# Kernel tuning notes

Hardware: AMD Instinct MI355X
Metric: run time of the kernel (lower is better)

Reference implementation:

```python
import jax, jax.numpy as jnp
import numpy as np
import math

GAMMA = 0.97      # discounting
LAM = 0.95        # gae lambda
EPSILON = 0.3     # ppo clip
EPS = 0.2         # gpo clip (eps)
ENT_COST = 0.01
RSCALE = 1.0
ALPHA = 1.0
NUM_STEPS = 1.0e6 # normalization step count buffer


def _mlp(x, Ws, bs):
    for i, (W, b) in enumerate(zip(Ws, bs)):
        x = x @ W.T + b
        if i < len(Ws) - 1:
            x = jax.nn.silu(x)
    return x


def _dist_create(logits):
    loc, s = jnp.split(logits, 2, axis=-1)
    return loc, jax.nn.softplus(s) + 0.001


def _log_det_jac(x):
    # tanh bijector log|det J| per element
    return 2.0 * (math.log(2.0) - x - jax.nn.softplus(-2.0 * x))


def _log_prob(loc, scale, dist):
    lu = -0.5 * jnp.square((dist - loc) / scale)
    ln = 0.5 * math.log(2.0 * math.pi) + jnp.log(scale)
    return (lu - ln - _log_det_jac(dist)).sum(-1)


def _entropy(loc, scale, noise):
    ln = 0.5 * math.log(2.0 * math.pi) + jnp.log(scale)
    ent = (0.5 + ln) * jnp.ones_like(loc)
    dist = loc + scale * noise  # reparameterized sample (torch.normal)
    return (ent + _log_det_jac(dist)).sum(-1)


def _kl(pl, ps, ql, qs):
    vr = jnp.square(ps / qs)
    t1 = jnp.square((pl - ql) / qs)
    return (0.5 * (vr + t1 - 1.0 - jnp.log(vr))).mean(-1)


def _normalize(obs, rm, rv):
    var = jnp.clip(rv / (NUM_STEPS + 1.0), 1e-6, 1e6)
    return jnp.clip((obs - rm) / jnp.sqrt(var), -5.0, 5.0)


def _gae(truncation, termination, reward, values, bootstrap_value):
    tm = 1.0 - truncation
    v1 = jnp.concatenate([values[1:], bootstrap_value[None]], 0)
    deltas = (reward + GAMMA * (1.0 - termination) * v1 - values) * tm

    def step(acc, xs):
        d, te, tmask = xs
        acc = d + GAMMA * (1.0 - te) * tmask * LAM * acc
        return acc, acc

    _, vmx = jax.lax.scan(step, jnp.zeros_like(bootstrap_value),
                          (deltas, termination, tm), reverse=True)
    vs = vmx + values
    vs1 = jnp.concatenate([vs[1:], bootstrap_value[None]], 0)
    adv = (reward + GAMMA * (1.0 - termination) * vs1 - values) * tm
    return vs, adv


def _loss(observation, pobservation, reward, done, truncation, logits, action,
          noise, pw0, pb0, pw1, pb1, pw2, pb2, vw0, vb0, vw1, vb1, vw2, vb2,
          running_mean, running_variance, kl_coef):
    sg = jax.lax.stop_gradient
    Pw, Pb = [pw0, pw1, pw2], [pb0, pb1, pb2]
    Vw, Vb = [vw0, vw1, vw2], [vb0, vb1, vb2]

    obs_n = _normalize(observation, running_mean, running_variance)
    pobs_n = _normalize(pobservation, running_mean, running_variance)

    guider_logits = _mlp(obs_n[:-1], Pw, Pb)
    learner_logits = _mlp(pobs_n[:-1], Pw, Pb)
    baseline = _mlp(obs_n, Vw, Vb).squeeze(-1)  # [T+1, B]
    bootstrap = baseline[-1]
    baseline = baseline[:-1]

    reward_s = reward * RSCALE
    termination = done * (1.0 - truncation)

    loc, scale = _dist_create(logits)
    b_lp = _log_prob(loc, scale, action)
    gl, gs = _dist_create(guider_logits)
    g_lp = _log_prob(gl, gs, action)
    ll, ls = _dist_create(learner_logits)
    l_lp = _log_prob(ll, ls, action)

    kl_learner = _kl(sg(gl), sg(gs), ll, ls).mean()
    kl_guider = _kl(gl, gs, sg(ll), sg(ls))
    # use_clip = True branch
    diff = g_lp - l_lp
    m = jnp.where(diff > math.log(1.0 + EPS), 1.0,
                  jnp.where(diff < math.log(1.0 - EPS), 1.0, 0.0))
    kl_guider = (kl_guider * m).mean()

    vs, adv = _gae(truncation, termination, reward_s, sg(baseline), sg(bootstrap))
    vs = sg(vs)
    adv = sg((adv - adv.mean()) / (jnp.std(adv, ddof=1) + 1e-5))

    rho = jnp.exp(g_lp - b_lp)
    rho_clip = jnp.exp(jnp.clip(g_lp - sg(l_lp), math.log(1.0 - EPS), math.log(1.0 + EPS))
                       + sg(l_lp) - b_lp)
    rho_clip = jnp.clip(rho_clip, 1.0 - EPSILON, 1.0 + EPSILON)
    guider_policy_loss = -jnp.mean(jnp.minimum(rho * adv, rho_clip * adv))

    rho2 = jnp.exp(jnp.minimum(l_lp - b_lp, 10.0))  # stable_exp
    rho2c = jnp.clip(rho2, 1.0 - EPSILON, 1.0 + EPSILON)
    learner_policy_loss = -jnp.mean(jnp.minimum(rho2 * adv, rho2c * adv))

    v_err = vs - baseline
    v_loss = jnp.mean(v_err * v_err) * 0.25

    entropy = jnp.mean(_entropy(loc, scale, noise))
    entropy_loss = -ENT_COST * entropy

    learner_loss = kl_learner + learner_policy_loss * ALPHA  # use_clip
    guider_loss = kl_guider + guider_policy_loss
    total = learner_loss + guider_loss + v_loss + entropy_loss
    return total, guider_loss, learner_loss, kl_learner


def setup_inputs() -> dict:
    key = jax.random.key(0)
    T, B, OBS, ACT, H = 1024, 256, 64, 8, 256
    ks = iter(jax.random.split(key, 32))

    def lin(fin, fout):
        W = jax.random.normal(next(ks), (fout, fin), jnp.float32) / np.float32(np.sqrt(fin))
        b = jnp.zeros((fout,), jnp.float32)
        return W, b

    pw0, pb0 = lin(OBS, H); pw1, pb1 = lin(H, H); pw2, pb2 = lin(H, 2 * ACT)
    vw0, vb0 = lin(OBS, H); vw1, vb1 = lin(H, H); vw2, vb2 = lin(H, 1)

    observation = jax.random.normal(next(ks), (T + 1, B, OBS), jnp.float32)
    pobservation = observation + 0.1 * jax.random.normal(next(ks), (T + 1, B, OBS), jnp.float32)
    reward = jax.random.normal(next(ks), (T, B), jnp.float32)
    done = (jax.random.uniform(next(ks), (T, B)) < 0.01).astype(jnp.float32)
    truncation = (jax.random.uniform(next(ks), (T, B)) < 0.005).astype(jnp.float32)
    logits = 0.5 * jax.random.normal(next(ks), (T, B, 2 * ACT), jnp.float32)
    action = jax.random.normal(next(ks), (T, B, ACT), jnp.float32)
    noise = jax.random.normal(next(ks), (T, B, ACT), jnp.float32)
    running_mean = jnp.zeros((OBS,), jnp.float32)
    running_variance = jnp.ones((OBS,), jnp.float32) * NUM_STEPS  # unit variance after /num_steps
    kl_coef = jnp.ones((1,), jnp.float32)

    return {"observation": observation, "pobservation": pobservation,
            "reward": reward, "done": done, "truncation": truncation,
            "logits": logits, "action": action, "noise": noise,
            "pw0": pw0, "pb0": pb0, "pw1": pw1, "pb1": pb1, "pw2": pw2, "pb2": pb2,
            "vw0": vw0, "vb0": vb0, "vw1": vw1, "vb1": vb1, "vw2": vw2, "vb2": vb2,
            "running_mean": running_mean, "running_variance": running_variance,
            "kl_coef": kl_coef}


def reference(observation, pobservation, reward, done, truncation, logits, action,
              noise, pw0, pb0, pw1, pb1, pw2, pb2, vw0, vb0, vw1, vb1, vw2, vb2,
              running_mean, running_variance, kl_coef):
    return _loss(observation, pobservation, reward, done, truncation, logits,
                 action, noise, pw0, pb0, pw1, pb1, pw2, pb2, vw0, vb0, vw1, vb1,
                 vw2, vb2, running_mean, running_variance, kl_coef)
```

## Files before the change

### kernel.cpp

```cpp
#include <hip/hip_runtime.h>
#include <math.h>

#define GAMMA_   0.97f
#define LAM_     0.95f
#define EPSILON_ 0.3f
#define HLOG2PI_ 0.91893853320467274f
#define LOG2C_   0.69314718055994531f
#define LOG1P2_  0.18232155679395463f
#define LOG0P8_  (-0.22314355131420976f)

typedef unsigned short u16;
typedef unsigned int   u32;
typedef _Float16 half8 __attribute__((ext_vector_type(8)));
typedef _Float16 half4 __attribute__((ext_vector_type(4)));
typedef __attribute__((ext_vector_type(4))) float floatx4;
typedef __attribute__((ext_vector_type(8))) float floatx8;

constexpr int  TT     = 1024;
constexpr long ROWS_P = (long)TT * 256;
constexpr long ROWS_V = (long)(TT + 1) * 256;

constexpr long FR_W0P_HI = 0;
constexpr long FR_W0P_LO = 16384;
constexpr long FR_W1P_HI = 32768;
// ... 14 lines not shown
constexpr long WS_BASE = WS_ADV + ROWS_P;
constexpr long WS_GA   = WS_BASE + ROWS_V;
constexpr long WS_GP   = WS_GA + 8192;
constexpr long WS_GS   = WS_GP + 8192;
constexpr long WS_BANK = WS_GS + 8192;


__device__ __forceinline__ float softplus_f(float x) {
  return (x > 20.f) ? x : log1pf(expf(x));
}
__device__ __forceinline__ float silu_f(float x) {
  return x * __builtin_amdgcn_rcpf(1.f + __expf(-x));
}
__device__ __forceinline__ float clamp30(float x) {
  return fminf(1e30f, fmaxf(-1e30f, x));
}

__global__ void prep_kernel(const float* __restrict__ rv,
                            float* __restrict__ inv_std,
                            float* __restrict__ accum,
                            float* __restrict__ accumB) {
  int t = threadIdx.x;
  if (t < 32) accum[t] = 0.f;
  accumB[t] = 0.f;
  if (t < 64) {
    float var = rv[t] / 1000001.0f;
    var = fminf(1e6f, fmaxf(1e-6f, var));
    inv_std[t] = 1.f / sqrtf(var);
  }
}

__global__ void convert_kernel(const float* __restrict__ pw0,
                               const float* __restrict__ pw1,
                               const float* __restrict__ pw2,
                               const float* __restrict__ vw0,
                               const float* __restrict__ vw1,
                               const float* __restrict__ vw2,
                               u16* __restrict__ frag) {
  int idx = blockIdx.x * 256 + threadIdx.x;
  const float* W; int kslog, K, nvalid; long hioff, looff; int e;
  if (idx < 16384)       { W = pw0; e = idx;          kslog = 1; K = 64;  nvalid = 256; hioff = FR_W0P_HI; looff = FR_W0P_LO; }
  else if (idx < 81920)  { W = pw1; e = idx - 16384;  kslog = 3; K = 256; nvalid = 256; hioff = FR_W1P_HI; looff = FR_W1P_LO; }
  else if (idx < 86016)  { W = pw2; e = idx - 81920;  kslog = 3; K = 256; nvalid = 16;  hioff = FR_W2P_HI; looff = FR_W2P_LO; }
  else if (idx < 102400) { W = vw0; e = idx - 86016;  kslog = 1; K = 64;  nvalid = 256; hioff = FR_W0V_HI; looff = FR_W0V_LO; }
  else if (idx < 167936) { W = vw1; e = idx - 102400; kslog = 3; K = 256; nvalid = 256; hioff = FR_W1V_HI; looff = FR_W1V_LO; }
  else                   { W = vw2; e = idx - 167936; kslog = 3; K = 256; nvalid = 1;   hioff = FR_W2V_HI; looff = FR_W2V_LO; }
  int j    = e & 7;
  int lane = (e >> 3) & 63;
  int ks   = (e >> 9) & ((1 << kslog) - 1);
  int nt   = e >> (9 + kslog);
  int n = nt * 16 + (lane & 15);
  int k = ks * 32 + ((lane >> 4) << 3) + j;
  float w = (n < nvalid) ? W[n * K + k] : 0.f;
  _Float16 hi = (_Float16)w;
  _Float16 lo = (_Float16)(w - (float)hi);
  frag[hioff + e] = *(u16*)&hi;
  frag[looff + e] = *(u16*)&lo;
}

constexpr int SX = 72;
constexpr int SH = 264;

__global__ __launch_bounds__(256, 3)
void policy_kernel(const float* __restrict__ obs,
                   const float* __restrict__ pobs,
                   const float* __restrict__ rm,
                   const float* __restrict__ inv_std,
                   const u16* __restrict__ frag,
                   const float* __restrict__ b0,
                   const float* __restrict__ b1,
                   const float* __restrict__ b2,
                   const float* __restrict__ logits,
                   const float* __restrict__ action,
                   const float* __restrict__ noise,
                   const float* __restrict__ adv,
                   const float* __restrict__ accum,
                   float* __restrict__ accumB) {
  __shared__ __align__(16) _Float16 H[64 * SH];
  __shared__ __align__(16) float OUTT[64 * 16];
  __shared__ float red[160];

  const int tid  = threadIdx.x;
  const long row0 = (long)blockIdx.x * 32;
  const int lane = tid & 63;
  const int wv   = tid >> 6;
  const int lm   = lane & 15;
  const int lq   = lane >> 4;

  _Float16* X = H;

  #pragma unroll
  for (int it = 0; it < 2; ++it) {
    int flat = it * 256 + tid;
    int vr = flat >> 3;
    int f0 = (flat & 7) * 8;
    const float* src = (vr < 32) ? obs : pobs;
    floatx8 v  = *(const floatx8*)&src[(row0 + (vr & 31)) * 64 + f0];
    floatx8 m  = *(const floatx8*)&rm[f0];
    floatx8 is = *(const floatx8*)&inv_std[f0];
    half8 h;
    #pragma unroll
    for (int j = 0; j < 8; ++j)
      h[j] = (_Float16)fminf(5.f, fmaxf(-5.f, (v[j] - m[j]) * is[j]));
    *(half8*)&X[vr * SX + f0] = h;
  }

  const int  er   = tid >> 3;
  const int  ed   = tid & 7;
  const long erow = row0 + er;
  float pf_a   = action[erow * 8 + ed];
  float pf_loc = logits[erow * 16 + ed];
  float pf_sr  = logits[erow * 16 + 8 + ed];
  float pf_nd  = noise[erow * 8 + ed];
  float pf_adv = adv[erow];
  float pf_s3  = accum[3];
  float pf_s4  = accum[4];

  const half8* B0h = (const half8*)(frag + FR_W0P_HI);
  const half8* B0l = (const half8*)(frag + FR_W0P_LO);
  half8 B0hr[2][4], B0lr[2][4];
  #pragma unroll
  for (int ks = 0; ks < 2; ++ks)
    #pragma unroll
    for (int nt = 0; nt < 4; ++nt) {
      int ntg = wv * 4 + nt;
      B0hr[ks][nt] = B0h[(ntg * 2 + ks) * 64 + lane];
      B0lr[ks][nt] = B0l[(ntg * 2 + ks) * 64 + lane];
    }
  __syncthreads();

  floatx4 acc[4][4];

  #pragma unroll
  for (int mt = 0; mt < 4; ++mt)
    #pragma unroll
    for (int nt = 0; nt < 4; ++nt) acc[mt][nt] = (floatx4){0.f,0.f,0.f,0.f};
  #pragma unroll
  for (int ks = 0; ks < 2; ++ks) {
    half8 A[4];
    #pragma unroll
    for (int mt = 0; mt < 4; ++mt)
      A[mt] = *(const half8*)&X[(mt * 16 + lm) * SX + ks * 32 + lq * 8];
    __builtin_amdgcn_s_setprio(1);
    #pragma unroll
    for (int mt = 0; mt < 4; ++mt)
      #pragma unroll
      for (int nt = 0; nt < 4; ++nt)
        acc[mt][nt] = __builtin_amdgcn_mfma_f32_16x16x32_f16(B0hr[ks][nt], A[mt], acc[mt][nt], 0, 0, 0);
    #pragma unroll
    for (int mt = 0; mt < 4; ++mt)
      #pragma unroll
      for (int nt = 0; nt < 4; ++nt)
        acc[mt][nt] = __builtin_amdgcn_mfma_f32_16x16x32_f16(B0lr[ks][nt], A[mt], acc[mt][nt], 0, 0, 0);
    __builtin_amdgcn_s_setprio(0);
  }

  const half8* B1h = (const half8*)(frag + FR_W1P_HI);
  const half8* B1l = (const half8*)(frag + FR_W1P_LO);
  half8 Bh[4], Bl[4], Bhn[4], Bln[4];
  #pragma unroll
  for (int nt = 0; nt < 4; ++nt) {
    int ntg = wv * 4 + nt;
    Bh[nt] = B1h[(ntg * 8) * 64 + lane];
    Bl[nt] = B1l[(ntg * 8) * 64 + lane];
  }

  __syncthreads();
  #pragma unroll
  for (int nt = 0; nt < 4; ++nt) {
    int colbase = (wv * 4 + nt) * 16 + lq * 4;
    floatx4 bias = *(const floatx4*)&b0[colbase];
    #pragma unroll
    for (int mt = 0; mt < 4; ++mt) {
      int row = mt * 16 + lm;
      half4 h;
      #pragma unroll
      for (int reg = 0; reg < 4; ++reg)
        h[reg] = (_Float16)silu_f(acc[mt][nt][reg] + bias[reg]);
      *(half4*)&H[row * SH + colbase] = h;
    }
  }
  __syncthreads();

  #pragma unroll
  for (int mt = 0; mt < 4; ++mt)
    #pragma unroll
    for (int nt = 0; nt < 4; ++nt) acc[mt][nt] = (floatx4){0.f,0.f,0.f,0.f};
  #pragma unroll 1
  for (int ks = 0; ks < 8; ++ks) {
    if (ks < 7) {
      #pragma unroll
      for (int nt = 0; nt < 4; ++nt) {
        int ntg = wv * 4 + nt;
        Bhn[nt] = B1h[(ntg * 8 + ks + 1) * 64 + lane];
        Bln[nt] = B1l[(ntg * 8 + ks + 1) * 64 + lane];
      }
    }
    half8 A[4];
    #pragma unroll
    for (int mt = 0; mt < 4; ++mt)
      A[mt] = *(const half8*)&H[(mt * 16 + lm) * SH + ks * 32 + lq * 8];
    __builtin_amdgcn_s_setprio(1);
    #pragma unroll
    for (int mt = 0; mt < 4; ++mt)
      #pragma unroll
      for (int nt = 0; nt < 4; ++nt)
        acc[mt][nt] = __builtin_amdgcn_mfma_f32_16x16x32_f16(Bh[nt], A[mt], acc[mt][nt], 0, 0, 0);
    #pragma unroll
    for (int mt = 0; mt < 4; ++mt)
      #pragma unroll
      for (int nt = 0; nt < 4; ++nt)
        acc[mt][nt] = __builtin_amdgcn_mfma_f32_16x16x32_f16(Bl[nt], A[mt], acc[mt][nt], 0, 0, 0);
    __builtin_amdgcn_s_setprio(0);
    if (ks < 7) {
      #pragma unroll
      for (int nt = 0; nt < 4; ++nt) { Bh[nt] = Bhn[nt]; Bl[nt] = Bln[nt]; }
    }
  }

  const half8* B2h = (const half8*)(frag + FR_W2P_HI);
  const half8* B2l = (const half8*)(frag + FR_W2P_LO);
  half8 B2hr[8], B2lr[8];
  #pragma unroll
  for (int ks = 0; ks < 8; ++ks) {
    B2hr[ks] = B2h[ks * 64 + lane];
    B2lr[ks] = B2l[ks * 64 + lane];
  }

  __syncthreads();
  #pragma unroll
  for (int nt = 0; nt < 4; ++nt) {
    int colbase = (wv * 4 + nt) * 16 + lq * 4;
    floatx4 bias = *(const floatx4*)&b1[colbase];
    #pragma unroll
    for (int mt = 0; mt < 4; ++mt) {
      int row = mt * 16 + lm;
      half4 h;
      #pragma unroll
      for (int reg = 0; reg < 4; ++reg)
        h[reg] = (_Float16)silu_f(acc[mt][nt][reg] + bias[reg]);
      *(half4*)&H[row * SH + colbase] = h;
    }
  }
  __syncthreads();

  {
    floatx4 c3a = (floatx4){0.f,0.f,0.f,0.f};
    floatx4 c3b = (floatx4){0.f,0.f,0.f,0.f};
    __builtin_amdgcn_s_setprio(1);
    #pragma unroll
    for (int ks = 0; ks < 8; ks += 2) {
      half8 A0 = *(const half8*)&H[(wv * 16 + lm) * SH + ks * 32 + lq * 8];
      half8 A1 = *(const half8*)&H[(wv * 16 + lm) * SH + (ks + 1) * 32 + lq * 8];
      c3a = __builtin_amdgcn_mfma_f32_16x16x32_f16(B2hr[ks],     A0, c3a, 0, 0, 0);
      c3b = __builtin_amdgcn_mfma_f32_16x16x32_f16(B2hr[ks + 1], A1, c3b, 0, 0, 0);
      c3a = __builtin_amdgcn_mfma_f32_16x16x32_f16(B2lr[ks],     A0, c3a, 0, 0, 0);
      c3b = __builtin_amdgcn_mfma_f32_16x16x32_f16(B2lr[ks + 1], A1, c3b, 0, 0, 0);
    }
    __builtin_amdgcn_s_setprio(0);
    floatx4 bias = *(const floatx4*)&b2[lq * 4];
    *(floatx4*)&OUTT[(wv * 16 + lm) * 16 + lq * 4] = c3a + c3b + bias;
  }
  __syncthreads();

  {
    int r = er;
    int d = ed;

    float gl  = OUTT[r * 16 + d];
    float gsr = OUTT[r * 16 + 8 + d];
    float ll  = OUTT[(32 + r) * 16 + d];
    float lsr = OUTT[(32 + r) * 16 + 8 + d];
    float a   = pf_a;
    float loc = pf_loc;
    float sr  = pf_sr;
    float nd  = pf_nd;

    float gs = softplus_f(gsr) + 1e-3f;
    float ls = softplus_f(lsr) + 1e-3f;
    float sc = softplus_f(sr) + 1e-3f;
    float ldj = 2.f * (LOG2C_ - a - softplus_f(-2.f * a));
    float lgs = logf(gs), lls = logf(ls), lsc = logf(sc);
    float zg = (a - gl) / gs;
    float zl = (a - ll) / ls;
    float z  = (a - loc) / sc;
    float glp = -0.5f * zg * zg - lgs - HLOG2PI_ - ldj;
    float llp = -0.5f * zl * zl - lls - HLOG2PI_ - ldj;
    float blp = -0.5f * z * z - lsc - HLOG2PI_ - ldj;
    float ratio = gs / ls;
    float vr = ratio * ratio;
    float t1 = (gl - ll) / ls; t1 *= t1;
    float kl = 0.5f * (vr + t1 - 1.f) - (lgs - lls);
    float dist = loc + sc * nd;
    float ent = 0.5f + HLOG2PI_ + lsc
              + 2.f * (LOG2C_ - dist - softplus_f(-2.f * dist));
// ... 12 lines not shown
      kl  = clamp30(kl);
      ent = clamp30(ent);

      float diff = glp - llp;
      float m = (diff > LOG1P2_ || diff < LOG0P8_) ? 1.f : 0.f;

      float N = (float)ROWS_P;
      float sum = pf_s3, sumsq = pf_s4;
      float mean = sum / N;
      float var  = fmaxf((sumsq - sum * sum / N) / (N - 1.f), 0.f);
      float inv  = 1.f / (sqrtf(var) + 1e-5f);
      float a_n  = (pf_adv - mean) * inv;

      float rho = expf(fminf(glp - blp, 80.f));
      float cl  = fminf(LOG1P2_, fmaxf(LOG0P8_, diff));
      float rc  = expf(fminf(cl + llp - blp, 80.f));
      rc = fminf(1.f + EPSILON_, fmaxf(1.f - EPSILON_, rc));
      float gp = clamp30(fminf(rho * a_n, rc * a_n));

      float rho2 = expf(fminf(llp - blp, 10.f));
      float r2c  = fminf(1.f + EPSILON_, fmaxf(1.f - EPSILON_, rho2));
      float lp = clamp30(fminf(rho2 * a_n, r2c * a_n));

      red[r]       = kl;
      red[32 + r]  = kl * m;
      red[64 + r]  = ent;
      red[96 + r]  = gp;
      red[128 + r] = lp;
    }
  }
  __syncthreads();
  if (tid < 32) {
    float s0 = red[tid], s1 = red[32 + tid], s2 = red[64 + tid];
    float s3 = red[96 + tid], s4 = red[128 + tid];
    #pragma unroll
    for (int o = 16; o > 0; o >>= 1) {
      s0 += __shfl_down(s0, o, 32);
      s1 += __shfl_down(s1, o, 32);
      s2 += __shfl_down(s2, o, 32);
      s3 += __shfl_down(s3, o, 32);
      s4 += __shfl_down(s4, o, 32);
    }
    if (tid == 0) {
      float* bank = accumB + (blockIdx.x & 31) * 8;
      atomicAdd(&bank[0], s0);
      atomicAdd(&bank[1], s1);
      atomicAdd(&bank[2], s2);
      atomicAdd(&bank[6], s3);
      atomicAdd(&bank[7], s4);
    }
  }
}

__global__ __launch_bounds__(256, 3)
void value_kernel(const float* __restrict__ obs,
                  const float* __restrict__ rm,
                  const float* __restrict__ inv_std,
                  const u16* __restrict__ frag,
                  const float* __restrict__ b0,
                  const float* __restrict__ b1,
                  const float* __restrict__ b2,
                  float* __restrict__ baseline) {
  __shared__ __align__(16) _Float16 H[64 * SH];

  const int tid  = threadIdx.x;
  const long row0 = (long)blockIdx.x * 64;
  const int lane = tid & 63;
  const int wv   = tid >> 6;
  const int lm   = lane & 15;
  const int lq   = lane >> 4;

  _Float16* X = H;

  #pragma unroll
  for (int it = 0; it < 2; ++it) {
    int flat = it * 256 + tid;
    int vr = flat >> 3;
    int f0 = (flat & 7) * 8;
    floatx8 v  = *(const floatx8*)&obs[(row0 + vr) * 64 + f0];
    floatx8 m  = *(const floatx8*)&rm[f0];
    floatx8 is = *(const floatx8*)&inv_std[f0];
    half8 h;
    #pragma unroll
    for (int j = 0; j < 8; ++j)
      h[j] = (_Float16)fminf(5.f, fmaxf(-5.f, (v[j] - m[j]) * is[j]));
    *(half8*)&X[vr * SX + f0] = h;
  }

  const half8* B0h = (const half8*)(frag + FR_W0V_HI);
  const half8* B0l = (const half8*)(frag + FR_W0V_LO);
  half8 B0hr[2][4], B0lr[2][4];
  #pragma unroll
  for (int ks = 0; ks < 2; ++ks)
    #pragma unroll
    for (int nt = 0; nt < 4; ++nt) {
      int ntg = wv * 4 + nt;
      B0hr[ks][nt] = B0h[(ntg * 2 + ks) * 64 + lane];
      B0lr[ks][nt] = B0l[(ntg * 2 + ks) * 64 + lane];
    }
  __syncthreads();

  floatx4 acc[4][4];

  #pragma unroll
  for (int mt = 0; mt < 4; ++mt)
    #pragma unroll
    for (int nt = 0; nt < 4; ++nt) acc[mt][nt] = (floatx4){0.f,0.f,0.f,0.f};
  #pragma unroll
  for (int ks = 0; ks < 2; ++ks) {
    half8 A[4];
    #pragma unroll
    for (int mt = 0; mt < 4; ++mt)
      A[mt] = *(const half8*)&X[(mt * 16 + lm) * SX + ks * 32 + lq * 8];
    __builtin_amdgcn_s_setprio(1);
    #pragma unroll
    for (int mt = 0; mt < 4; ++mt)
      #pragma unroll
      for (int nt = 0; nt < 4; ++nt)
        acc[mt][nt] = __builtin_amdgcn_mfma_f32_16x16x32_f16(B0hr[ks][nt], A[mt], acc[mt][nt], 0, 0, 0);
    #pragma unroll
    for (int mt = 0; mt < 4; ++mt)
      #pragma unroll
      for (int nt = 0; nt < 4; ++nt)
        acc[mt][nt] = __builtin_amdgcn_mfma_f32_16x16x32_f16(B0lr[ks][nt], A[mt], acc[mt][nt], 0, 0, 0);
    __builtin_amdgcn_s_setprio(0);
  }

  const half8* B1h = (const half8*)(frag + FR_W1V_HI);
  const half8* B1l = (const half8*)(frag + FR_W1V_LO);
  half8 Bh[4], Bl[4], Bhn[4], Bln[4];
  #pragma unroll
  for (int nt = 0; nt < 4; ++nt) {
    int ntg = wv * 4 + nt;
    Bh[nt] = B1h[(ntg * 8) * 64 + lane];
    Bl[nt] = B1l[(ntg * 8) * 64 + lane];
  }

  __syncthreads();
  #pragma unroll
  for (int nt = 0; nt < 4; ++nt) {
    int colbase = (wv * 4 + nt) * 16 + lq * 4;
    floatx4 bias = *(const floatx4*)&b0[colbase];
    #pragma unroll
    for (int mt = 0; mt < 4; ++mt) {
      int row = mt * 16 + lm;
      half4 h;
      #pragma unroll
      for (int reg = 0; reg < 4; ++reg)
        h[reg] = (_Float16)silu_f(acc[mt][nt][reg] + bias[reg]);
      *(half4*)&H[row * SH + colbase] = h;
    }
  }
  __syncthreads();

  #pragma unroll
  for (int mt = 0; mt < 4; ++mt)
    #pragma unroll
    for (int nt = 0; nt < 4; ++nt) acc[mt][nt] = (floatx4){0.f,0.f,0.f,0.f};
  #pragma unroll 1
  for (int ks = 0; ks < 8; ++ks) {
    if (ks < 7) {
      #pragma unroll
      for (int nt = 0; nt < 4; ++nt) {
        int ntg = wv * 4 + nt;
        Bhn[nt] = B1h[(ntg * 8 + ks + 1) * 64 + lane];
        Bln[nt] = B1l[(ntg * 8 + ks + 1) * 64 + lane];
      }
    }
    half8 A[4];
    #pragma unroll
    for (int mt = 0; mt < 4; ++mt)
      A[mt] = *(const half8*)&H[(mt * 16 + lm) * SH + ks * 32 + lq * 8];
    __builtin_amdgcn_s_setprio(1);
    #pragma unroll
    for (int mt = 0; mt < 4; ++mt)
      #pragma unroll
      for (int nt = 0; nt < 4; ++nt)
        acc[mt][nt] = __builtin_amdgcn_mfma_f32_16x16x32_f16(Bh[nt], A[mt], acc[mt][nt], 0, 0, 0);
    #pragma unroll
    for (int mt = 0; mt < 4; ++mt)
      #pragma unroll
      for (int nt = 0; nt < 4; ++nt)
        acc[mt][nt] = __builtin_amdgcn_mfma_f32_16x16x32_f16(Bl[nt], A[mt], acc[mt][nt], 0, 0, 0);
    __builtin_amdgcn_s_setprio(0);
    if (ks < 7) {
      #pragma unroll
      for (int nt = 0; nt < 4; ++nt) { Bh[nt] = Bhn[nt]; Bl[nt] = Bln[nt]; }
    }
  }

  const half8* B2h = (const half8*)(frag + FR_W2V_HI);
  const half8* B2l = (const half8*)(frag + FR_W2V_LO);
  half8 B2hr[8], B2lr[8];
  #pragma unroll
  for (int ks = 0; ks < 8; ++ks) {
    B2hr[ks] = B2h[ks * 64 + lane];
    B2lr[ks] = B2l[ks * 64 + lane];
  }

  __syncthreads();
  #pragma unroll
  for (int nt = 0; nt < 4; ++nt) {
    int colbase = (wv * 4 + nt) * 16 + lq * 4;
    floatx4 bias = *(const floatx4*)&b1[colbase];
    #pragma unroll
    for (int mt = 0; mt < 4; ++mt) {
      int row = mt * 16 + lm;
      half4 h;
      #pragma unroll
      for (int reg = 0; reg < 4; ++reg)
        h[reg] = (_Float16)silu_f(acc[mt][nt][reg] + bias[reg]);
      *(half4*)&H[row * SH + colbase] = h;
    }
  }
  __syncthreads();

  {
    floatx4 c3a = (floatx4){0.f,0.f,0.f,0.f};
    floatx4 c3b = (floatx4){0.f,0.f,0.f,0.f};
    __builtin_amdgcn_s_setprio(1);
    #pragma unroll
    for (int ks = 0; ks < 8; ks += 2) {
      half8 A0 = *(const half8*)&H[(wv * 16 + lm) * SH + ks * 32 + lq * 8];
      half8 A1 = *(const half8*)&H[(wv * 16 + lm) * SH + (ks + 1) * 32 + lq * 8];
      c3a = __builtin_amdgcn_mfma_f32_16x16x32_f16(B2hr[ks],     A0, c3a, 0, 0, 0);
      c3b = __builtin_amdgcn_mfma_f32_16x16x32_f16(B2hr[ks + 1], A1, c3b, 0, 0, 0);
      c3a = __builtin_amdgcn_mfma_f32_16x16x32_f16(B2lr[ks],     A0, c3a, 0, 0, 0);
      c3b = __builtin_amdgcn_mfma_f32_16x16x32_f16(B2lr[ks + 1], A1, c3b, 0, 0, 0);
    }
    __builtin_amdgcn_s_setprio(0);
    if (lq == 0) baseline[row0 + wv * 16 + lm] = c3a[0] + c3b[0] + b2[0];
  }
}

__global__ void gae_phase1(const float* __restrict__ reward,
                           const float* __restrict__ done,
                           const float* __restrict__ trunc,
                           const float* __restrict__ baseline,
                           float* __restrict__ A, float* __restrict__ P) {
  int s = blockIdx.x, b = threadIdx.x;
  float Aa = 0.f, Pp = 1.f;
  for (int t = (s + 1) * 32 - 1; t >= s * 32; --t) {
    int idx = t * 256 + b;
    float r = reward[idx], d = done[idx], tr = trunc[idx];
    float tm = 1.f - tr;
    float te = d * tm;
    float bl = baseline[idx], bl1 = baseline[idx + 256];
    float g1 = GAMMA_ * (1.f - te);
    float delta = (r + g1 * bl1 - bl) * tm;
    float c = g1 * tm * LAM_;
    Aa = delta + c * Aa;
    Pp = c * Pp;
  }
  A[s * 256 + b] = Aa;
  P[s * 256 + b] = Pp;
// ... 46 lines not shown
  for (int o = 32; o > 0; o >>= 1) {
    v0 += __shfl_down(v0, o, 64);
    v1 += __shfl_down(v1, o, 64);
    v2 += __shfl_down(v2, o, 64);
  }
  int lane = threadIdx.x & 63, w = threadIdx.x >> 6;
  if (lane == 0) { red[w] = v0; red[4 + w] = v1; red[8 + w] = v2; }
  __syncthreads();
  if (threadIdx.x == 0) {
    float s0=0.f, s1=0.f, s2=0.f;
    for (int q = 0; q < 4; ++q) { s0 += red[q]; s1 += red[4+q]; s2 += red[8+q]; }
    atomicAdd(&accum[3], s0);
    atomicAdd(&accum[4], s1);
    atomicAdd(&accum[5], s2);
  }
}

__global__ void finalize_kernel(const float* __restrict__ accum,
                                const float* __restrict__ accumB,
                                float* __restrict__ out) {
  int t = threadIdx.x;
  float s0 = 0.f, s1 = 0.f, s2 = 0.f, s6 = 0.f, s7 = 0.f;
  if (t < 32) {
    const float* bank = accumB + t * 8;
    s0 = bank[0]; s1 = bank[1]; s2 = bank[2]; s6 = bank[6]; s7 = bank[7];
  }
  #pragma unroll
  for (int o = 16; o > 0; o >>= 1) {
    s0 += __shfl_down(s0, o, 64);
    s1 += __shfl_down(s1, o, 64);
    s2 += __shfl_down(s2, o, 64);
    s6 += __shfl_down(s6, o, 64);
    s7 += __shfl_down(s7, o, 64);
  }
  if (t == 0) {
    float N = (float)ROWS_P;
    float kl_learner = s0 / N;
    float kl_guider  = s1 / N;
    float entropy    = s2 / N;
    float v_loss     = 0.25f * accum[5] / N;
    float gp_loss    = -s6 / N;
    float lp_loss    = -s7 / N;
    float learner_loss = kl_learner + lp_loss;
    float guider_loss  = kl_guider + gp_loss;
    float total = learner_loss + guider_loss + v_loss - 0.01f * entropy;
    out[0] = total;
    out[1] = guider_loss;
// ... 24 lines not shown
  const float* vb0 = (const float*)d_in[15];
  const float* vw1 = (const float*)d_in[16];
  const float* vb1 = (const float*)d_in[17];
  const float* vw2 = (const float*)d_in[18];
  const float* vb2 = (const float*)d_in[19];
  const float* rm  = (const float*)d_in[20];
  const float* rv  = (const float*)d_in[21];

  u16*   frag  = (u16*)d_ws;
  float* fbase = (float*)d_ws + FR_TOTAL / 2;
  float* accum   = fbase + WS_ACC;
  float* inv_std = fbase + WS_INV;
  float* adv     = fbase + WS_ADV;
  float* base    = fbase + WS_BASE;
  float* gA      = fbase + WS_GA;
  float* gP      = fbase + WS_GP;
  float* gS      = fbase + WS_GS;
  float* accumB  = fbase + WS_BANK;
  float* out = (float*)d_out;

  prep_kernel<<<1, 256, 0, stream>>>(rv, inv_std, accum, accumB);
  convert_kernel<<<672, 256, 0, stream>>>(pw0, pw1, pw2, vw0, vw1, vw2, frag);

  value_kernel<<<(int)(ROWS_V / 64), 256, 0, stream>>>(
      obs, rm, inv_std, frag, vb0, vb1, vb2, base);

  gae_phase1<<<32, 256, 0, stream>>>(reward, done, trunc, base, gA, gP);
  gae_phase2<<<1, 256, 0, stream>>>(gA, gP, gS);
  gae_phase3<<<32, 256, 0, stream>>>(reward, done, trunc, base, gS, adv, accum);

  policy_kernel<<<(int)(ROWS_P / 32), 256, 0, stream>>>(
      obs, pobs, rm, inv_std, frag, pb0, pb1, pb2,
      logits, action, noise, adv, accum, accumB);

  finalize_kernel<<<1, 64, 0, stream>>>(accum, accumB, out);
}
```

Measured before the change: 504.2 us.

## Halve per-block row tile in MLP kernels to raise occupancy and cut registers

Both the value and policy MLP kernels now process half as many rows per block (32 instead of 64 M-rows), which halves the accumulator and LDS footprint. Launch bounds rise from 3 to 5 blocks per SIMD to exploit this. Weight fragments are now streamed per k-step instead of being held in registers or double-buffered, and biases are folded into the accumulator initialisation. The final layer splits K across wave pairs with an LDS reduction. Reduction banks are padded to 32 floats to spread atomics across addresses. In exchange, each weight fragment is fetched from global/L2 twice as often per row and there are more blocks and atomics.

Result: slower. 583.9 us (+15.8%).

```diff
diff --git a/kernel.cpp b/kernel.cpp
--- a/kernel.cpp
+++ b/kernel.cpp
@@ -60,7 +60,7 @@
                             float* __restrict__ accumB) {
   int t = threadIdx.x;
   if (t < 32) accum[t] = 0.f;
-  accumB[t] = 0.f;
+  for (int i = t; i < 1024; i += 256) accumB[i] = 0.f;
   if (t < 64) {
     float var = rv[t] / 1000001.0f;
     var = fminf(1e6f, fmaxf(1e-6f, var));
@@ -99,7 +99,7 @@
 constexpr int SX = 72;
 constexpr int SH = 264;
 
-__global__ __launch_bounds__(256, 3)
+__global__ __launch_bounds__(256, 5)
 void policy_kernel(const float* __restrict__ obs,
                    const float* __restrict__ pobs,
                    const float* __restrict__ rm,
@@ -114,12 +114,12 @@
                    const float* __restrict__ adv,
                    const float* __restrict__ accum,
                    float* __restrict__ accumB) {
-  __shared__ __align__(16) _Float16 H[64 * SH];
-  __shared__ __align__(16) float OUTT[64 * 16];
-  __shared__ float red[160];
+  __shared__ __align__(16) _Float16 H[32 * SH];
+  __shared__ __align__(16) float OUT2[2 * 32 * 16];
+  __shared__ float red[80];
 
   const int tid  = threadIdx.x;
-  const long row0 = (long)blockIdx.x * 32;
+  const long row0 = (long)blockIdx.x * 16;
   const int lane = tid & 63;
   const int wv   = tid >> 6;
   const int lm   = lane & 15;
@@ -127,13 +127,11 @@
 
   _Float16* X = H;
 
-  #pragma unroll
-  for (int it = 0; it < 2; ++it) {
-    int flat = it * 256 + tid;
-    int vr = flat >> 3;
-    int f0 = (flat & 7) * 8;
-    const float* src = (vr < 32) ? obs : pobs;
-    floatx8 v  = *(const floatx8*)&src[(row0 + (vr & 31)) * 64 + f0];
+  {
+    int vr = tid >> 3;
+    int f0 = (tid & 7) * 8;
+    const float* src = (vr < 16) ? obs : pobs;
+    floatx8 v  = *(const floatx8*)&src[(row0 + (vr & 15)) * 64 + f0];
     floatx8 m  = *(const floatx8*)&rm[f0];
     floatx8 is = *(const floatx8*)&inv_std[f0];
     half8 h;
@@ -143,7 +141,7 @@
     *(half8*)&X[vr * SX + f0] = h;
   }
 
-  const int  er   = tid >> 3;
+  const int  er   = (tid >> 3) & 15;
   const int  ed   = tid & 7;
   const long erow = row0 + er;
   float pf_a   = action[erow * 8 + ed];
@@ -154,161 +152,139 @@
   float pf_s3  = accum[3];
   float pf_s4  = accum[4];
 
-  const half8* B0h = (const half8*)(frag + FR_W0P_HI);
-  const half8* B0l = (const half8*)(frag + FR_W0P_LO);
-  half8 B0hr[2][4], B0lr[2][4];
-  #pragma unroll
-  for (int ks = 0; ks < 2; ++ks)
-    #pragma unroll
-    for (int nt = 0; nt < 4; ++nt) {
-      int ntg = wv * 4 + nt;
-      B0hr[ks][nt] = B0h[(ntg * 2 + ks) * 64 + lane];
-      B0lr[ks][nt] = B0l[(ntg * 2 + ks) * 64 + lane];
-    }
-  __syncthreads();
-
-  floatx4 acc[4][4];
-
-  #pragma unroll
-  for (int mt = 0; mt < 4; ++mt)
-    #pragma unroll
-    for (int nt = 0; nt < 4; ++nt) acc[mt][nt] = (floatx4){0.f,0.f,0.f,0.f};
-  #pragma unroll
-  for (int ks = 0; ks < 2; ++ks) {
-    half8 A[4];
-    #pragma unroll
-    for (int mt = 0; mt < 4; ++mt)
-      A[mt] = *(const half8*)&X[(mt * 16 + lm) * SX + ks * 32 + lq * 8];
-    __builtin_amdgcn_s_setprio(1);
-    #pragma unroll
-    for (int mt = 0; mt < 4; ++mt)
-      #pragma unroll
-      for (int nt = 0; nt < 4; ++nt)
-        acc[mt][nt] = __builtin_amdgcn_mfma_f32_16x16x32_f16(B0hr[ks][nt], A[mt], acc[mt][nt], 0, 0, 0);
-    #pragma unroll
-    for (int mt = 0; mt < 4; ++mt)
-      #pragma unroll
-      for (int nt = 0; nt < 4; ++nt)
-        acc[mt][nt] = __builtin_amdgcn_mfma_f32_16x16x32_f16(B0lr[ks][nt], A[mt], acc[mt][nt], 0, 0, 0);
-    __builtin_amdgcn_s_setprio(0);
-  }
-
-  const half8* B1h = (const half8*)(frag + FR_W1P_HI);
-  const half8* B1l = (const half8*)(frag + FR_W1P_LO);
-  half8 Bh[4], Bl[4], Bhn[4], Bln[4];
+  floatx4 acc[2][4];
   #pragma unroll
   for (int nt = 0; nt < 4; ++nt) {
-    int ntg = wv * 4 + nt;
-    Bh[nt] = B1h[(ntg * 8) * 64 + lane];
-    Bl[nt] = B1l[(ntg * 8) * 64 + lane];
-  }
-
-  __syncthreads();
+    floatx4 bz = *(const floatx4*)&b0[(wv * 4 + nt) * 16 + lq * 4];
+    acc[0][nt] = bz; acc[1][nt] = bz;
+  }
+  __syncthreads();
+
+  {
+    const half8* B0h = (const half8*)(frag + FR_W0P_HI);
+    const half8* B0l = (const half8*)(frag + FR_W0P_LO);
+    #pragma unroll
+    for (int ks = 0; ks < 2; ++ks) {
+      half8 Bh[4], Bl[4];
+      #pragma unroll
+      for (int nt = 0; nt < 4; ++nt) {
+        int ntg = wv * 4 + nt;
+        Bh[nt] = B0h[(ntg * 2 + ks) * 64 + lane];
+        Bl[nt] = B0l[(ntg * 2 + ks) * 64 + lane];
+      }
+      half8 A0 = *(const half8*)&X[lm * SX + ks * 32 + lq * 8];
+      half8 A1 = *(const half8*)&X[(16 + lm) * SX + ks * 32 + lq * 8];
+      __builtin_amdgcn_s_setprio(1);
+      #pragma unroll
+      for (int nt = 0; nt < 4; ++nt) {
+        acc[0][nt] = __builtin_amdgcn_mfma_f32_16x16x32_f16(Bh[nt], A0, acc[0][nt], 0, 0, 0);
+        acc[1][nt] = __builtin_amdgcn_mfma_f32_16x16x32_f16(Bh[nt], A1, acc[1][nt], 0, 0, 0);
+      }
+      #pragma unroll
+      for (int nt = 0; nt < 4; ++nt) {
+        acc[0][nt] = __builtin_amdgcn_mfma_f32_16x16x32_f16(Bl[nt], A0, acc[0][nt], 0, 0, 0);
+        acc[1][nt] = __builtin_amdgcn_mfma_f32_16x16x32_f16(Bl[nt], A1, acc[1][nt], 0, 0, 0);
+      }
+      __builtin_amdgcn_s_setprio(0);
+    }
+  }
+  __syncthreads();
+
   #pragma unroll
   for (int nt = 0; nt < 4; ++nt) {
     int colbase = (wv * 4 + nt) * 16 + lq * 4;
-    floatx4 bias = *(const floatx4*)&b0[colbase];
-    #pragma unroll
-    for (int mt = 0; mt < 4; ++mt) {
+    #pragma unroll
+    for (int mt = 0; mt < 2; ++mt) {
       int row = mt * 16 + lm;
       half4 h;
       #pragma unroll
       for (int reg = 0; reg < 4; ++reg)
-        h[reg] = (_Float16)silu_f(acc[mt][nt][reg] + bias[reg]);
+        h[reg] = (_Float16)silu_f(acc[mt][nt][reg]);
       *(half4*)&H[row * SH + colbase] = h;
     }
   }
   __syncthreads();
 
-  #pragma unroll
-  for (int mt = 0; mt < 4; ++mt)
-    #pragma unroll
-    for (int nt = 0; nt < 4; ++nt) acc[mt][nt] = (floatx4){0.f,0.f,0.f,0.f};
-  #pragma unroll 1
-  for (int ks = 0; ks < 8; ++ks) {
-    if (ks < 7) {
+  {
+    const half8* B1h = (const half8*)(frag + FR_W1P_HI);
+    const half8* B1l = (const half8*)(frag + FR_W1P_LO);
+    #pragma unroll
+    for (int nt = 0; nt < 4; ++nt) {
+      floatx4 bz = *(const floatx4*)&b1[(wv * 4 + nt) * 16 + lq * 4];
+      acc[0][nt] = bz; acc[1][nt] = bz;
+    }
+    #pragma unroll 1
+    for (int ks = 0; ks < 8; ++ks) {
+      half8 Bh[4], Bl[4];
       #pragma unroll
       for (int nt = 0; nt < 4; ++nt) {
         int ntg = wv * 4 + nt;
-        Bhn[nt] = B1h[(ntg * 8 + ks + 1) * 64 + lane];
-        Bln[nt] = B1l[(ntg * 8 + ks + 1) * 64 + lane];
-      }
-    }
-    half8 A[4];
-    #pragma unroll
-    for (int mt = 0; mt < 4; ++mt)
-      A[mt] = *(const half8*)&H[(mt * 16 + lm) * SH + ks * 32 + lq * 8];
-    __builtin_amdgcn_s_setprio(1);
-    #pragma unroll
-    for (int mt = 0; mt < 4; ++mt)
-      #pragma unroll
-      for (int nt = 0; nt < 4; ++nt)
-        acc[mt][nt] = __builtin_amdgcn_mfma_f32_16x16x32_f16(Bh[nt], A[mt], acc[mt][nt], 0, 0, 0);
-    #pragma unroll
-    for (int mt = 0; mt < 4; ++mt)
-      #pragma unroll
-      for (int nt = 0; nt < 4; ++nt)
-        acc[mt][nt] = __builtin_amdgcn_mfma_f32_16x16x32_f16(Bl[nt], A[mt], acc[mt][nt], 0, 0, 0);
-    __builtin_amdgcn_s_setprio(0);
-    if (ks < 7) {
-      #pragma unroll
-      for (int nt = 0; nt < 4; ++nt) { Bh[nt] = Bhn[nt]; Bl[nt] = Bln[nt]; }
-    }
-  }
-
-  const half8* B2h = (const half8*)(frag + FR_W2P_HI);
-  const half8* B2l = (const half8*)(frag + FR_W2P_LO);
-  half8 B2hr[8], B2lr[8];
-  #pragma unroll
-  for (int ks = 0; ks < 8; ++ks) {
-    B2hr[ks] = B2h[ks * 64 + lane];
-    B2lr[ks] = B2l[ks * 64 + lane];
-  }
-
-  __syncthreads();
+        Bh[nt] = B1h[(ntg * 8 + ks) * 64 + lane];
+        Bl[nt] = B1l[(ntg * 8 + ks) * 64 + lane];
+      }
+      half8 A0 = *(const half8*)&H[lm * SH + ks * 32 + lq * 8];
+      half8 A1 = *(const half8*)&H[(16 + lm) * SH + ks * 32 + lq * 8];
+      __builtin_amdgcn_s_setprio(1);
+      #pragma unroll
+      for (int nt = 0; nt < 4; ++nt) {
+        acc[0][nt] = __builtin_amdgcn_mfma_f32_16x16x32_f16(Bh[nt], A0, acc[0][nt], 0, 0, 0);
+        acc[1][nt] = __builtin_amdgcn_mfma_f32_16x16x32_f16(Bh[nt], A1, acc[1][nt], 0, 0, 0);
+      }
+      #pragma unroll
+      for (int nt = 0; nt < 4; ++nt) {
+        acc[0][nt] = __builtin_amdgcn_mfma_f32_16x16x32_f16(Bl[nt], A0, acc[0][nt], 0, 0, 0);
+        acc[1][nt] = __builtin_amdgcn_mfma_f32_16x16x32_f16(Bl[nt], A1, acc[1][nt], 0, 0, 0);
+      }
+      __builtin_amdgcn_s_setprio(0);
+    }
+  }
+  __syncthreads();
+
   #pragma unroll
   for (int nt = 0; nt < 4; ++nt) {
     int colbase = (wv * 4 + nt) * 16 + lq * 4;
-    floatx4 bias = *(const floatx4*)&b1[colbase];
-    #pragma unroll
-    for (int mt = 0; mt < 4; ++mt) {
+    #pragma unroll
+    for (int mt = 0; mt < 2; ++mt) {
       int row = mt * 16 + lm;
       half4 h;
       #pragma unroll
       for (int reg = 0; reg < 4; ++reg)
-        h[reg] = (_Float16)silu_f(acc[mt][nt][reg] + bias[reg]);
+        h[reg] = (_Float16)silu_f(acc[mt][nt][reg]);
       *(half4*)&H[row * SH + colbase] = h;
     }
   }
   __syncthreads();
 
   {
-    floatx4 c3a = (floatx4){0.f,0.f,0.f,0.f};
-    floatx4 c3b = (floatx4){0.f,0.f,0.f,0.f};
+    const half8* B2h = (const half8*)(frag + FR_W2P_HI);
+    const half8* B2l = (const half8*)(frag + FR_W2P_LO);
+    const int m3 = wv & 1, kh = wv >> 1;
+    floatx4 c3a, c3b = (floatx4){0.f, 0.f, 0.f, 0.f};
+    c3a = (kh == 0) ? *(const floatx4*)&b2[lq * 4] : (floatx4){0.f, 0.f, 0.f, 0.f};
     __builtin_amdgcn_s_setprio(1);
     #pragma unroll
-    for (int ks = 0; ks < 8; ks += 2) {
-      half8 A0 = *(const half8*)&H[(wv * 16 + lm) * SH + ks * 32 + lq * 8];
-      half8 A1 = *(const half8*)&H[(wv * 16 + lm) * SH + (ks + 1) * 32 + lq * 8];
-      c3a = __builtin_amdgcn_mfma_f32_16x16x32_f16(B2hr[ks],     A0, c3a, 0, 0, 0);
-      c3b = __builtin_amdgcn_mfma_f32_16x16x32_f16(B2hr[ks + 1], A1, c3b, 0, 0, 0);
-      c3a = __builtin_amdgcn_mfma_f32_16x16x32_f16(B2lr[ks],     A0, c3a, 0, 0, 0);
-      c3b = __builtin_amdgcn_mfma_f32_16x16x32_f16(B2lr[ks + 1], A1, c3b, 0, 0, 0);
+    for (int j = 0; j < 4; j += 2) {
+      int ks = kh * 4 + j;
+      half8 A0 = *(const half8*)&H[(m3 * 16 + lm) * SH + ks * 32 + lq * 8];
+      half8 A1 = *(const half8*)&H[(m3 * 16 + lm) * SH + (ks + 1) * 32 + lq * 8];
+      c3a = __builtin_amdgcn_mfma_f32_16x16x32_f16(B2h[ks * 64 + lane],       A0, c3a, 0, 0, 0);
+      c3b = __builtin_amdgcn_mfma_f32_16x16x32_f16(B2h[(ks + 1) * 64 + lane], A1, c3b, 0, 0, 0);
+      c3a = __builtin_amdgcn_mfma_f32_16x16x32_f16(B2l[ks * 64 + lane],       A0, c3a, 0, 0, 0);
+      c3b = __builtin_amdgcn_mfma_f32_16x16x32_f16(B2l[(ks + 1) * 64 + lane], A1, c3b, 0, 0, 0);
     }
     __builtin_amdgcn_s_setprio(0);
-    floatx4 bias = *(const floatx4*)&b2[lq * 4];
-    *(floatx4*)&OUTT[(wv * 16 + lm) * 16 + lq * 4] = c3a + c3b + bias;
-  }
-  __syncthreads();
-
-  {
-    int r = er;
-    int d = ed;
-
-    float gl  = OUTT[r * 16 + d];
-    float gsr = OUTT[r * 16 + 8 + d];
-    float ll  = OUTT[(32 + r) * 16 + d];
-    float lsr = OUTT[(32 + r) * 16 + 8 + d];
+    *(floatx4*)&OUT2[kh * 512 + (m3 * 16 + lm) * 16 + lq * 4] = c3a + c3b;
+  }
+  __syncthreads();
+
+  if (tid < 128) {
+    int r = tid >> 3;
+    int d = tid & 7;
+
+    float gl  = OUT2[r * 16 + d]            + OUT2[512 + r * 16 + d];
+    float gsr = OUT2[r * 16 + 8 + d]        + OUT2[512 + r * 16 + 8 + d];
+    float ll  = OUT2[(16 + r) * 16 + d]     + OUT2[512 + (16 + r) * 16 + d];
+    float lsr = OUT2[(16 + r) * 16 + 8 + d] + OUT2[512 + (16 + r) * 16 + 8 + d];
     float a   = pf_a;
     float loc = pf_loc;
     float sr  = pf_sr;
@@ -367,27 +343,27 @@
       float r2c  = fminf(1.f + EPSILON_, fmaxf(1.f - EPSILON_, rho2));
       float lp = clamp30(fminf(rho2 * a_n, r2c * a_n));
 
-      red[r]       = kl;
-      red[32 + r]  = kl * m;
-      red[64 + r]  = ent;
-      red[96 + r]  = gp;
-      red[128 + r] = lp;
-    }
-  }
-  __syncthreads();
-  if (tid < 32) {
-    float s0 = red[tid], s1 = red[32 + tid], s2 = red[64 + tid];
-    float s3 = red[96 + tid], s4 = red[128 + tid];
-    #pragma unroll
-    for (int o = 16; o > 0; o >>= 1) {
-      s0 += __shfl_down(s0, o, 32);
-      s1 += __shfl_down(s1, o, 32);
-      s2 += __shfl_down(s2, o, 32);
-      s3 += __shfl_down(s3, o, 32);
-      s4 += __shfl_down(s4, o, 32);
+      red[r]      = kl;
+      red[16 + r] = kl * m;
+      red[32 + r] = ent;
+      red[48 + r] = gp;
+      red[64 + r] = lp;
+    }
+  }
+  __syncthreads();
+  if (tid < 16) {
+    float s0 = red[tid], s1 = red[16 + tid], s2 = red[32 + tid];
+    float s3 = red[48 + tid], s4 = red[64 + tid];
+    #pragma unroll
+    for (int o = 8; o > 0; o >>= 1) {
+      s0 += __shfl_down(s0, o, 16);
+      s1 += __shfl_down(s1, o, 16);
+      s2 += __shfl_down(s2, o, 16);
+      s3 += __shfl_down(s3, o, 16);
+      s4 += __shfl_down(s4, o, 16);
     }
     if (tid == 0) {
-      float* bank = accumB + (blockIdx.x & 31) * 8;
+      float* bank = accumB + (blockIdx.x & 31) * 32;
       atomicAdd(&bank[0], s0);
       atomicAdd(&bank[1], s1);
       atomicAdd(&bank[2], s2);
@@ -397,7 +373,7 @@
   }
 }
 
-__global__ __launch_bounds__(256, 3)
+__global__ __launch_bounds__(256, 5)
 void value_kernel(const float* __restrict__ obs,
                   const float* __restrict__ rm,
                   const float* __restrict__ inv_std,
@@ -406,10 +382,11 @@
                   const float* __restrict__ b1,
                   const float* __restrict__ b2,
                   float* __restrict__ baseline) {
-  __shared__ __align__(16) _Float16 H[64 * SH];
+  __shared__ __align__(16) _Float16 H[32 * SH];
+  __shared__ float OUT2V[64];
 
   const int tid  = threadIdx.x;
-  const long row0 = (long)blockIdx.x * 64;
+  const long row0 = (long)blockIdx.x * 32;
   const int lane = tid & 63;
   const int wv   = tid >> 6;
   const int lm   = lane & 15;
@@ -417,11 +394,9 @@
 
   _Float16* X = H;
 
-  #pragma unroll
-  for (int it = 0; it < 2; ++it) {
-    int flat = it * 256 + tid;
-    int vr = flat >> 3;
-    int f0 = (flat & 7) * 8;
+  {
+    int vr = tid >> 3;
+    int f0 = (tid & 7) * 8;
     floatx8 v  = *(const floatx8*)&obs[(row0 + vr) * 64 + f0];
     floatx8 m  = *(const floatx8*)&rm[f0];
     floatx8 is = *(const floatx8*)&inv_std[f0];
@@ -432,150 +407,133 @@
     *(half8*)&X[vr * SX + f0] = h;
   }
 
-  const half8* B0h = (const half8*)(frag + FR_W0V_HI);
-  const half8* B0l = (const half8*)(frag + FR_W0V_LO);
-  half8 B0hr[2][4], B0lr[2][4];
-  #pragma unroll
-  for (int ks = 0; ks < 2; ++ks)
-    #pragma unroll
-    for (int nt = 0; nt < 4; ++nt) {
-      int ntg = wv * 4 + nt;
-      B0hr[ks][nt] = B0h[(ntg * 2 + ks) * 64 + lane];
-      B0lr[ks][nt] = B0l[(ntg * 2 + ks) * 64 + lane];
-    }
-  __syncthreads();
-
-  floatx4 acc[4][4];
-
-  #pragma unroll
-  for (int mt = 0; mt < 4; ++mt)
-    #pragma unroll
-    for (int nt = 0; nt < 4; ++nt) acc[mt][nt] = (floatx4){0.f,0.f,0.f,0.f};
-  #pragma unroll
-  for (int ks = 0; ks < 2; ++ks) {
-    half8 A[4];
-    #pragma unroll
-    for (int mt = 0; mt < 4; ++mt)
-      A[mt] = *(const half8*)&X[(mt * 16 + lm) * SX + ks * 32 + lq * 8];
-    __builtin_amdgcn_s_setprio(1);
-    #pragma unroll
-    for (int mt = 0; mt < 4; ++mt)
-      #pragma unroll
-      for (int nt = 0; nt < 4; ++nt)
-        acc[mt][nt] = __builtin_amdgcn_mfma_f32_16x16x32_f16(B0hr[ks][nt], A[mt], acc[mt][nt], 0, 0, 0);
-    #pragma unroll
-    for (int mt = 0; mt < 4; ++mt)
-      #pragma unroll
-      for (int nt = 0; nt < 4; ++nt)
-        acc[mt][nt] = __builtin_amdgcn_mfma_f32_16x16x32_f16(B0lr[ks][nt], A[mt], acc[mt][nt], 0, 0, 0);
-    __builtin_amdgcn_s_setprio(0);
-  }
-
-  const half8* B1h = (const half8*)(frag + FR_W1V_HI);
-  const half8* B1l = (const half8*)(frag + FR_W1V_LO);
-  half8 Bh[4], Bl[4], Bhn[4], Bln[4];
+  floatx4 acc[2][4];
   #pragma unroll
   for (int nt = 0; nt < 4; ++nt) {
-    int ntg = wv * 4 + nt;
-    Bh[nt] = B1h[(ntg * 8) * 64 + lane];
-    Bl[nt] = B1l[(ntg * 8) * 64 + lane];
-  }
-
-  __syncthreads();
+    floatx4 bz = *(const floatx4*)&b0[(wv * 4 + nt) * 16 + lq * 4];
+    acc[0][nt] = bz; acc[1][nt] = bz;
+  }
+  __syncthreads();
+
+  {
+    const half8* B0h = (const half8*)(frag + FR_W0V_HI);
+    const half8* B0l = (const half8*)(frag + FR_W0V_LO);
+    #pragma unroll
+    for (int ks = 0; ks < 2; ++ks) {
+      half8 Bh[4], Bl[4];
+      #pragma unroll
+      for (int nt = 0; nt < 4; ++nt) {
+        int ntg = wv * 4 + nt;
+        Bh[nt] = B0h[(ntg * 2 + ks) * 64 + lane];
+        Bl[nt] = B0l[(ntg * 2 + ks) * 64 + lane];
+      }
+      half8 A0 = *(const half8*)&X[lm * SX + ks * 32 + lq * 8];
+      half8 A1 = *(const half8*)&X[(16 + lm) * SX + ks * 32 + lq * 8];
+      __builtin_amdgcn_s_setprio(1);
+      #pragma unroll
+      for (int nt = 0; nt < 4; ++nt) {
+        acc[0][nt] = __builtin_amdgcn_mfma_f32_16x16x32_f16(Bh[nt], A0, acc[0][nt], 0, 0, 0);
+        acc[1][nt] = __builtin_amdgcn_mfma_f32_16x16x32_f16(Bh[nt], A1, acc[1][nt], 0, 0, 0);
+      }
+      #pragma unroll
+      for (int nt = 0; nt < 4; ++nt) {
+        acc[0][nt] = __builtin_amdgcn_mfma_f32_16x16x32_f16(Bl[nt], A0, acc[0][nt], 0, 0, 0);
+        acc[1][nt] = __builtin_amdgcn_mfma_f32_16x16x32_f16(Bl[nt], A1, acc[1][nt], 0, 0, 0);
+      }
+      __builtin_amdgcn_s_setprio(0);
+    }
+  }
+  __syncthreads();
+
   #pragma unroll
   for (int nt = 0; nt < 4; ++nt) {
     int colbase = (wv * 4 + nt) * 16 + lq * 4;
-    floatx4 bias = *(const floatx4*)&b0[colbase];
-    #pragma unroll
-    for (int mt = 0; mt < 4; ++mt) {
+    #pragma unroll
+    for (int mt = 0; mt < 2; ++mt) {
       int row = mt * 16 + lm;
       half4 h;
       #pragma unroll
       for (int reg = 0; reg < 4; ++reg)
-        h[reg] = (_Float16)silu_f(acc[mt][nt][reg] + bias[reg]);
+        h[reg] = (_Float16)silu_f(acc[mt][nt][reg]);
       *(half4*)&H[row * SH + colbase] = h;
     }
   }
   __syncthreads();
 
-  #pragma unroll
-  for (int mt = 0; mt < 4; ++mt)
-    #pragma unroll
-    for (int nt = 0; nt < 4; ++nt) acc[mt][nt] = (floatx4){0.f,0.f,0.f,0.f};
-  #pragma unroll 1
-  for (int ks = 0; ks < 8; ++ks) {
-    if (ks < 7) {
+  {
+    const half8* B1h = (const half8*)(frag + FR_W1V_HI);
+    const half8* B1l = (const half8*)(frag + FR_W1V_LO);
+    #pragma unroll
+    for (int nt = 0; nt < 4; ++nt) {
+      floatx4 bz = *(const floatx4*)&b1[(wv * 4 + nt) * 16 + lq * 4];
+      acc[0][nt] = bz; acc[1][nt] = bz;
+    }
+    #pragma unroll 1
+    for (int ks = 0; ks < 8; ++ks) {
+      half8 Bh[4], Bl[4];
       #pragma unroll
       for (int nt = 0; nt < 4; ++nt) {
         int ntg = wv * 4 + nt;
-        Bhn[nt] = B1h[(ntg * 8 + ks + 1) * 64 + lane];
-        Bln[nt] = B1l[(ntg * 8 + ks + 1) * 64 + lane];
-      }
-    }
-    half8 A[4];
-    #pragma unroll
-    for (int mt = 0; mt < 4; ++mt)
-      A[mt] = *(const half8*)&H[(mt * 16 + lm) * SH + ks * 32 + lq * 8];
-    __builtin_amdgcn_s_setprio(1);
-    #pragma unroll
-    for (int mt = 0; mt < 4; ++mt)
-      #pragma unroll
-      for (int nt = 0; nt < 4; ++nt)
-        acc[mt][nt] = __builtin_amdgcn_mfma_f32_16x16x32_f16(Bh[nt], A[mt], acc[mt][nt], 0, 0, 0);
-    #pragma unroll
-    for (int mt = 0; mt < 4; ++mt)
-      #pragma unroll
-      for (int nt = 0; nt < 4; ++nt)
-        acc[mt][nt] = __builtin_amdgcn_mfma_f32_16x16x32_f16(Bl[nt], A[mt], acc[mt][nt], 0, 0, 0);
-    __builtin_amdgcn_s_setprio(0);
-    if (ks < 7) {
-      #pragma unroll
-      for (int nt = 0; nt < 4; ++nt) { Bh[nt] = Bhn[nt]; Bl[nt] = Bln[nt]; }
-    }
-  }
-
-  const half8* B2h = (const half8*)(frag + FR_W2V_HI);
-  const half8* B2l = (const half8*)(frag + FR_W2V_LO);
-  half8 B2hr[8], B2lr[8];
-  #pragma unroll
-  for (int ks = 0; ks < 8; ++ks) {
-    B2hr[ks] = B2h[ks * 64 + lane];
-    B2lr[ks] = B2l[ks * 64 + lane];
-  }
-
-  __syncthreads();
+        Bh[nt] = B1h[(ntg * 8 + ks) * 64 + lane];
+        Bl[nt] = B1l[(ntg * 8 + ks) * 64 + lane];
+      }
+      half8 A0 = *(const half8*)&H[lm * SH + ks * 32 + lq * 8];
+      half8 A1 = *(const half8*)&H[(16 + lm) * SH + ks * 32 + lq * 8];
+      __builtin_amdgcn_s_setprio(1);
+      #pragma unroll
+      for (int nt = 0; nt < 4; ++nt) {
+        acc[0][nt] = __builtin_amdgcn_mfma_f32_16x16x32_f16(Bh[nt], A0, acc[0][nt], 0, 0, 0);
+        acc[1][nt] = __builtin_amdgcn_mfma_f32_16x16x32_f16(Bh[nt], A1, acc[1][nt], 0, 0, 0);
+      }
+      #pragma unroll
+      for (int nt = 0; nt < 4; ++nt) {
+        acc[0][nt] = __builtin_amdgcn_mfma_f32_16x16x32_f16(Bl[nt], A0, acc[0][nt], 0, 0, 0);
+        acc[1][nt] = __builtin_amdgcn_mfma_f32_16x16x32_f16(Bl[nt], A1, acc[1][nt], 0, 0, 0);
+      }
+      __builtin_amdgcn_s_setprio(0);
+    }
+  }
+  __syncthreads();
+
   #pragma unroll
   for (int nt = 0; nt < 4; ++nt) {
     int colbase = (wv * 4 + nt) * 16 + lq * 4;
-    floatx4 bias = *(const floatx4*)&b1[colbase];
-    #pragma unroll
-    for (int mt = 0; mt < 4; ++mt) {
+    #pragma unroll
+    for (int mt = 0; mt < 2; ++mt) {
       int row = mt * 16 + lm;
       half4 h;
       #pragma unroll
       for (int reg = 0; reg < 4; ++reg)
-        h[reg] = (_Float16)silu_f(acc[mt][nt][reg] + bias[reg]);
+        h[reg] = (_Float16)silu_f(acc[mt][nt][reg]);
       *(half4*)&H[row * SH + colbase] = h;
     }
   }
   __syncthreads();
 
   {
-    floatx4 c3a = (floatx4){0.f,0.f,0.f,0.f};
-    floatx4 c3b = (floatx4){0.f,0.f,0.f,0.f};
+    const half8* B2h = (const half8*)(frag + FR_W2V_HI);
+    const half8* B2l = (const half8*)(frag + FR_W2V_LO);
+    const int m3 = wv & 1, kh = wv >> 1;
+    float bz = (kh == 0 && lq == 0) ? b2[0] : 0.f;
+    floatx4 c3a = (floatx4){bz, 0.f, 0.f, 0.f};
+    floatx4 c3b = (floatx4){0.f, 0.f, 0.f, 0.f};
     __builtin_amdgcn_s_setprio(1);
     #pragma unroll
-    for (int ks = 0; ks < 8; ks += 2) {
-      half8 A0 = *(const half8*)&H[(wv * 16 + lm) * SH + ks * 32 + lq * 8];
-      half8 A1 = *(const half8*)&H[(wv * 16 + lm) * SH + (ks + 1) * 32 + lq * 8];
-      c3a = __builtin_amdgcn_mfma_f32_16x16x32_f16(B2hr[ks],     A0, c3a, 0, 0, 0);
-      c3b = __builtin_amdgcn_mfma_f32_16x16x32_f16(B2hr[ks + 1], A1, c3b, 0, 0, 0);
-      c3a = __builtin_amdgcn_mfma_f32_16x16x32_f16(B2lr[ks],     A0, c3a, 0, 0, 0);
-      c3b = __builtin_amdgcn_mfma_f32_16x16x32_f16(B2lr[ks + 1], A1, c3b, 0, 0, 0);
+    for (int j = 0; j < 4; j += 2) {
+      int ks = kh * 4 + j;
+      half8 A0 = *(const half8*)&H[(m3 * 16 + lm) * SH + ks * 32 + lq * 8];
+      half8 A1 = *(const half8*)&H[(m3 * 16 + lm) * SH + (ks + 1) * 32 + lq * 8];
+      c3a = __builtin_amdgcn_mfma_f32_16x16x32_f16(B2h[ks * 64 + lane],       A0, c3a, 0, 0, 0);
+      c3b = __builtin_amdgcn_mfma_f32_16x16x32_f16(B2h[(ks + 1) * 64 + lane], A1, c3b, 0, 0, 0);
+      c3a = __builtin_amdgcn_mfma_f32_16x16x32_f16(B2l[ks * 64 + lane],       A0, c3a, 0, 0, 0);
+      c3b = __builtin_amdgcn_mfma_f32_16x16x32_f16(B2l[(ks + 1) * 64 + lane], A1, c3b, 0, 0, 0);
     }
     __builtin_amdgcn_s_setprio(0);
-    if (lq == 0) baseline[row0 + wv * 16 + lm] = c3a[0] + c3b[0] + b2[0];
-  }
+    if (lq == 0) OUT2V[kh * 32 + m3 * 16 + lm] = c3a[0] + c3b[0];
+  }
+  __syncthreads();
+
+  if (tid < 32) baseline[row0 + tid] = OUT2V[tid] + OUT2V[32 + tid];
 }
 
 __global__ void gae_phase1(const float* __restrict__ reward,
@@ -668,7 +626,7 @@
   int t = threadIdx.x;
   float s0 = 0.f, s1 = 0.f, s2 = 0.f, s6 = 0.f, s7 = 0.f;
   if (t < 32) {
-    const float* bank = accumB + t * 8;
+    const float* bank = accumB + t * 32;
     s0 = bank[0]; s1 = bank[1]; s2 = bank[2]; s6 = bank[6]; s7 = bank[7];
   }
   #pragma unroll
@@ -739,14 +697,14 @@
   prep_kernel<<<1, 256, 0, stream>>>(rv, inv_std, accum, accumB);
   convert_kernel<<<672, 256, 0, stream>>>(pw0, pw1, pw2, vw0, vw1, vw2, frag);
 
-  value_kernel<<<(int)(ROWS_V / 64), 256, 0, stream>>>(
+  value_kernel<<<(int)(ROWS_V / 32), 256, 0, stream>>>(
       obs, rm, inv_std, frag, vb0, vb1, vb2, base);
 
   gae_phase1<<<32, 256, 0, stream>>>(reward, done, trunc, base, gA, gP);
   gae_phase2<<<1, 256, 0, stream>>>(gA, gP, gS);
   gae_phase3<<<32, 256, 0, stream>>>(reward, done, trunc, base, gS, adv, accum);
 
-  policy_kernel<<<(int)(ROWS_P / 32), 256, 0, stream>>>(
+  policy_kernel<<<(int)(ROWS_P / 16), 256, 0, stream>>>(
       obs, pobs, rm, inv_std, frag, pb0, pb1, pb2,
       logits, action, noise, adv, accum, accumB);
 
```
